# Optimization experiments

Hardware: AMD Instinct MI355X
Metric: run time of the kernel (lower is better)

The kernel has to match this reference:

```python
import jax, jax.numpy as jnp
import numpy as np

COMMITMENT_WEIGHT = 0.25


def setup_inputs() -> dict:
    key = jax.random.key(0)
    k1, k2 = jax.random.split(key)
    embed_dim, codebook_size = 512, 16
    z = jax.random.normal(k1, (8, 8192, embed_dim), dtype=jnp.float32)
    # init matches nn.init.uniform_(-1/K, 1/K) scale; values are arbitrary for correctness testing
    codebook = jax.random.uniform(k2, (codebook_size, embed_dim), dtype=jnp.float32,
                                  minval=-1.0 / codebook_size, maxval=1.0 / codebook_size)
    return {"z": z, "codebook": codebook}


def reference(z, codebook):
    D = z.shape[-1]
    flat_z = z.reshape(-1, D)                                   # [N, D]
    # squared L2 distances via expansion: |z|^2 - 2 z.C^T + |c|^2   -> [N, K]
    distances = (jnp.sum(flat_z * flat_z, axis=1, keepdims=True)
                 - 2.0 * flat_z @ codebook.T
                 + jnp.sum(codebook * codebook, axis=1)[None, :])
    indices = jnp.argmin(distances, axis=1)                      # [N]
    z_q_flat = codebook[indices]                                 # [N, D] gather

    commitment_loss = jnp.mean((flat_z - jax.lax.stop_gradient(z_q_flat)) ** 2)
    codebook_loss = jnp.mean((z_q_flat - jax.lax.stop_gradient(flat_z)) ** 2)
    vq_loss = codebook_loss + COMMITMENT_WEIGHT * commitment_loss

    # straight-through estimator
    z_q_flat = flat_z + jax.lax.stop_gradient(z_q_flat - flat_z)
    z_q = z_q_flat.reshape(z.shape)
    indices = indices.reshape(z.shape[:-1])
    return (z_q, indices, vq_loss)
```

## Files before the change

kernel.cpp:

```cpp
#include <hip/hip_runtime.h>


constexpr int D      = 512;
constexpr int D4     = D / 4;
constexpr int K      = 16;
constexpr int BLOCK  = 256;
constexpr int WAVES  = BLOCK / 64;
constexpr int ROWS_PER_WAVE  = 4;
constexpr int ROWS_PER_BLOCK = WAVES * ROWS_PER_WAVE;
constexpr int GRID   = 2048;

__global__ void __launch_bounds__(BLOCK, 4) vq_kernel(
    const float* __restrict__ z, const float* __restrict__ cb,
    float* __restrict__ zq, float* __restrict__ idx_out,
    float* __restrict__ loss_out, int n_rows, float loss_scale)
{
    __shared__ float cb_lds[K * D];
    __shared__ float cnorm_lds[K];
    __shared__ float wave_loss[WAVES];

    const int tid  = threadIdx.x;
    const int lane = tid & 63;
    const int wave = tid >> 6;
    const int sub  = lane >> 4;
    const int sl   = lane & 15;

    const float4* cb4 = reinterpret_cast<const float4*>(cb);
    float4*       cl4 = reinterpret_cast<float4*>(cb_lds);
    #pragma unroll
    for (int i = 0; i < (K * D4) / BLOCK; ++i)
        cl4[i * BLOCK + tid] = cb4[i * BLOCK + tid];
    __syncthreads();

    {
        const int k = tid >> 4;
        const int s = tid & 15;
        double acc = 0.0;
        #pragma unroll
        for (int i = 0; i < 8; ++i) {
            float4 c = cl4[k * D4 + i * 16 + s];
            acc += (double)c.x * (double)c.x + (double)c.y * (double)c.y
                 + (double)c.z * (double)c.z + (double)c.w * (double)c.w;
        }
        #pragma unroll
        for (int m = 1; m < 16; m <<= 1)
            acc += __shfl_xor(acc, m, 64);
        if (s == 0) cnorm_lds[k] = (float)acc;
    }
    __syncthreads();

    const int base_k = sl & 3;
    float cn[4];
    #pragma unroll
    for (int c = 0; c < 4; ++c) cn[c] = cnorm_lds[4 * c + base_k];

    const float4* z4  = reinterpret_cast<const float4*>(z);
    float4*       zq4 = reinterpret_cast<float4*>(zq);

    float lp = 0.f;

    const int n_tiles = n_rows / ROWS_PER_BLOCK;
    for (int tile = blockIdx.x; tile < n_tiles; tile += GRID) {
        const int row = tile * ROWS_PER_BLOCK + wave * ROWS_PER_WAVE + sub;
        const long long rb = (long long)row * D4;

        float4 zr[8];
        #pragma unroll
        for (int i = 0; i < 8; ++i)
            zr[i] = z4[rb + i * 16 + sl];

        double A = 0.0;
        #pragma unroll
        for (int i = 0; i < 8; ++i) {
            A += (double)zr[i].x * (double)zr[i].x + (double)zr[i].y * (double)zr[i].y
               + (double)zr[i].z * (double)zr[i].z + (double)zr[i].w * (double)zr[i].w;
        }
        #pragma unroll
        for (int m = 1; m < 16; m <<= 1)
            A += __shfl_xor(A, m, 64);
        const float A32 = (float)A;

        float B32[4];
        #pragma unroll
        for (int c = 0; c < 4; ++c) {
            double a0 = 0.0, a1 = 0.0, a2 = 0.0, a3 = 0.0;
            #pragma unroll 1
            for (int i = 0; i < 8; ++i) {
                const int    idx = (4 * c) * D4 + i * 16 + sl;
                const double zx = (double)zr[i].x, zy = (double)zr[i].y;
                const double zz = (double)zr[i].z, zw = (double)zr[i].w;
                float4 c0 = cl4[idx];
                float4 c1 = cl4[idx + D4];
                float4 c2 = cl4[idx + 2 * D4];
                float4 c3 = cl4[idx + 3 * D4];
                a0 = fma((double)c0.x, zx, fma((double)c0.y, zy, fma((double)c0.z, zz, fma((double)c0.w, zw, a0))));
                a1 = fma((double)c1.x, zx, fma((double)c1.y, zy, fma((double)c1.z, zz, fma((double)c1.w, zw, a1))));
                a2 = fma((double)c2.x, zx, fma((double)c2.y, zy, fma((double)c2.z, zz, fma((double)c2.w, zw, a2))));
                a3 = fma((double)c3.x, zx, fma((double)c3.y, zy, fma((double)c3.z, zz, fma((double)c3.w, zw, a3))));
            }
            {
                const int mb0 = lane & 1;
                double s0 = mb0 ? a0 : a1;
                double s1 = mb0 ? a2 : a3;
                double r0 = __shfl_xor(s0, 1, 64);
                double r1 = __shfl_xor(s1, 1, 64);
                double t0 = (mb0 ? a1 : a0) + r0;
                double t1 = (mb0 ? a3 : a2) + r1;
                const int mb1 = (lane >> 1) & 1;
                double s2 = mb1 ? t0 : t1;
                double r2 = __shfl_xor(s2, 2, 64);
                double u  = (mb1 ? t1 : t0) + r2;
                u += __shfl_xor(u, 4, 64);
                u += __shfl_xor(u, 8, 64);
                B32[c] = (float)u;
            }
        }

        float bd = (A32 - 2.0f * B32[0]) + cn[0];
        int   bk = base_k;
        #pragma unroll
        for (int c = 1; c < 4; ++c) {
            float d = (A32 - 2.0f * B32[c]) + cn[c];
            if (d < bd) { bd = d; bk = 4 * c + base_k; }
        }
        #pragma unroll
        for (int b = 0; b < 2; ++b) {
            float od = __shfl_xor(bd, 1 << b, 64);
            int   ok = __shfl_xor(bk, 1 << b, 64);
            if (od < bd || (od == bd && ok < bk)) { bd = od; bk = ok; }
        }
        if (sl == 0) idx_out[row] = (float)bk;

        #pragma unroll
        for (int i = 0; i < 8; ++i) {
            float4 c = cl4[bk * D4 + i * 16 + sl];
            zq4[rb + i * 16 + sl] = c;
            float dx = zr[i].x - c.x, dy = zr[i].y - c.y;
            float dz = zr[i].z - c.z, dw = zr[i].w - c.w;
            lp += dx * dx + dy * dy + dz * dz + dw * dw;
        }
    }

    #pragma unroll
    for (int m = 1; m < 64; m <<= 1)
        lp += __shfl_xor(lp, m, 64);
    if (lane == 0) wave_loss[wave] = lp;
    __syncthreads();
    if (tid == 0) {
        float s = 0.f;
        #pragma unroll
        for (int w = 0; w < WAVES; ++w) s += wave_loss[w];
        atomicAdd(loss_out, s * loss_scale);
    }
}

extern "C" void kernel_launch(void* const* d_in, const int* in_sizes, int n_in,
                              void* d_out, int out_size, void* d_ws, size_t ws_size,
                              hipStream_t stream) {
    const float* z  = (const float*)d_in[0];
    const float* cb = (const float*)d_in[1];

    const int n_elems = in_sizes[0];
    const int n_rows  = n_elems / D;

    float* zq   = (float*)d_out;
    float* idx  = zq + n_elems;
    float* loss = idx + n_rows;

    hipMemsetAsync((void*)loss, 0, sizeof(float), stream);

    const float loss_scale = 1.25f / (float)n_elems;
    vq_kernel<<<GRID, BLOCK, 0, stream>>>(z, cb, zq, idx, loss, n_rows, loss_scale);
}
```

Baseline: 326.9 us.

## Use nontemporal loads/stores, per-wave norms, and drop block-level sync

Switches z loads and zq stores to nontemporal builtins so streaming traffic bypasses cache retention. Each wave now computes codebook norms itself and spreads them with shuffles, removing a shared array and one barrier. The final loss is added with one atomic per wave instead of a block reduction, and the dot-product loop unroll is raised to 2 with launch bounds raised to 5. The costs are four times more loss atomics and redundant norm work in every wave. Higher occupancy may not be reachable given the 32KB LDS per block.

```diff
diff --git a/kernel.cpp b/kernel.cpp
--- a/kernel.cpp
+++ b/kernel.cpp
@@ -1,23 +1,21 @@
 #include <hip/hip_runtime.h>
 
+
+typedef float f32x4 __attribute__((ext_vector_type(4)));
 
 constexpr int D      = 512;
 constexpr int D4     = D / 4;
 constexpr int K      = 16;
 constexpr int BLOCK  = 256;
-constexpr int WAVES  = BLOCK / 64;
-constexpr int ROWS_PER_WAVE  = 4;
-constexpr int ROWS_PER_BLOCK = WAVES * ROWS_PER_WAVE;
+constexpr int ROWS_PER_BLOCK = 16;
 constexpr int GRID   = 2048;
 
-__global__ void __launch_bounds__(BLOCK, 4) vq_kernel(
+__global__ void __launch_bounds__(BLOCK, 5) vq_kernel(
     const float* __restrict__ z, const float* __restrict__ cb,
     float* __restrict__ zq, float* __restrict__ idx_out,
     float* __restrict__ loss_out, int n_rows, float loss_scale)
 {
-    __shared__ float cb_lds[K * D];
-    __shared__ float cnorm_lds[K];
-    __shared__ float wave_loss[WAVES];
+    __shared__ f32x4 cb_lds4[K * D4];
 
     const int tid  = threadIdx.x;
     const int lane = tid & 63;
@@ -25,55 +23,54 @@
     const int sub  = lane >> 4;
     const int sl   = lane & 15;
 
-    const float4* cb4 = reinterpret_cast<const float4*>(cb);
-    float4*       cl4 = reinterpret_cast<float4*>(cb_lds);
+    const f32x4* cb4 = reinterpret_cast<const f32x4*>(cb);
     #pragma unroll
     for (int i = 0; i < (K * D4) / BLOCK; ++i)
-        cl4[i * BLOCK + tid] = cb4[i * BLOCK + tid];
+        cb_lds4[i * BLOCK + tid] = cb4[i * BLOCK + tid];
     __syncthreads();
 
+    float cn[4];
     {
-        const int k = tid >> 4;
-        const int s = tid & 15;
-        double acc = 0.0;
+        const int k_ = lane >> 2;
+        const int s_ = lane & 3;
+        double nacc = 0.0;
+        #pragma unroll 1
+        for (int j = 0; j < 32; ++j) {
+            const int jj = (j + 2 * k_) & 31;
+            f32x4 c = cb_lds4[k_ * D4 + jj * 4 + s_];
+            nacc += (double)c[0] * (double)c[0] + (double)c[1] * (double)c[1]
+                  + (double)c[2] * (double)c[2] + (double)c[3] * (double)c[3];
+        }
+        nacc += __shfl_xor(nacc, 1, 64);
+        nacc += __shfl_xor(nacc, 2, 64);
+        const float normf = (float)nacc;
+        const int base_k = sl & 3;
         #pragma unroll
-        for (int i = 0; i < 8; ++i) {
-            float4 c = cl4[k * D4 + i * 16 + s];
-            acc += (double)c.x * (double)c.x + (double)c.y * (double)c.y
-                 + (double)c.z * (double)c.z + (double)c.w * (double)c.w;
-        }
-        #pragma unroll
-        for (int m = 1; m < 16; m <<= 1)
-            acc += __shfl_xor(acc, m, 64);
-        if (s == 0) cnorm_lds[k] = (float)acc;
+        for (int c = 0; c < 4; ++c)
+            cn[c] = __shfl(normf, (4 * c + base_k) * 4, 64);
     }
-    __syncthreads();
+    const int base_k = sl & 3;
 
-    const int base_k = sl & 3;
-    float cn[4];
-    #pragma unroll
-    for (int c = 0; c < 4; ++c) cn[c] = cnorm_lds[4 * c + base_k];
-
-    const float4* z4  = reinterpret_cast<const float4*>(z);
-    float4*       zq4 = reinterpret_cast<float4*>(zq);
+    const f32x4* z4  = reinterpret_cast<const f32x4*>(z);
+    f32x4*       zq4 = reinterpret_cast<f32x4*>(zq);
 
     float lp = 0.f;
 
     const int n_tiles = n_rows / ROWS_PER_BLOCK;
     for (int tile = blockIdx.x; tile < n_tiles; tile += GRID) {
-        const int row = tile * ROWS_PER_BLOCK + wave * ROWS_PER_WAVE + sub;
+        const int row = tile * ROWS_PER_BLOCK + wave * 4 + sub;
         const long long rb = (long long)row * D4;
 
-        float4 zr[8];
+        f32x4 zr[8];
         #pragma unroll
         for (int i = 0; i < 8; ++i)
-            zr[i] = z4[rb + i * 16 + sl];
+            zr[i] = __builtin_nontemporal_load(&z4[rb + i * 16 + sl]);
 
         double A = 0.0;
         #pragma unroll
         for (int i = 0; i < 8; ++i) {
-            A += (double)zr[i].x * (double)zr[i].x + (double)zr[i].y * (double)zr[i].y
-               + (double)zr[i].z * (double)zr[i].z + (double)zr[i].w * (double)zr[i].w;
+            A += (double)zr[i][0] * (double)zr[i][0] + (double)zr[i][1] * (double)zr[i][1]
+               + (double)zr[i][2] * (double)zr[i][2] + (double)zr[i][3] * (double)zr[i][3];
         }
         #pragma unroll
         for (int m = 1; m < 16; m <<= 1)
@@ -84,19 +81,19 @@
         #pragma unroll
         for (int c = 0; c < 4; ++c) {
             double a0 = 0.0, a1 = 0.0, a2 = 0.0, a3 = 0.0;
-            #pragma unroll 1
+            #pragma unroll 2
             for (int i = 0; i < 8; ++i) {
                 const int    idx = (4 * c) * D4 + i * 16 + sl;
-                const double zx = (double)zr[i].x, zy = (double)zr[i].y;
-                const double zz = (double)zr[i].z, zw = (double)zr[i].w;
-                float4 c0 = cl4[idx];
-                float4 c1 = cl4[idx + D4];
-                float4 c2 = cl4[idx + 2 * D4];
-                float4 c3 = cl4[idx + 3 * D4];
-                a0 = fma((double)c0.x, zx, fma((double)c0.y, zy, fma((double)c0.z, zz, fma((double)c0.w, zw, a0))));
-                a1 = fma((double)c1.x, zx, fma((double)c1.y, zy, fma((double)c1.z, zz, fma((double)c1.w, zw, a1))));
-                a2 = fma((double)c2.x, zx, fma((double)c2.y, zy, fma((double)c2.z, zz, fma((double)c2.w, zw, a2))));
-                a3 = fma((double)c3.x, zx, fma((double)c3.y, zy, fma((double)c3.z, zz, fma((double)c3.w, zw, a3))));
+                const double zx = (double)zr[i][0], zy = (double)zr[i][1];
+                const double zz = (double)zr[i][2], zw = (double)zr[i][3];
+                f32x4 c0 = cb_lds4[idx];
+                f32x4 c1 = cb_lds4[idx + D4];
+                f32x4 c2 = cb_lds4[idx + 2 * D4];
+                f32x4 c3 = cb_lds4[idx + 3 * D4];
+                a0 = fma((double)c0[0], zx, fma((double)c0[1], zy, fma((double)c0[2], zz, fma((double)c0[3], zw, a0))));
+                a1 = fma((double)c1[0], zx, fma((double)c1[1], zy, fma((double)c1[2], zz, fma((double)c1[3], zw, a1))));
+                a2 = fma((double)c2[0], zx, fma((double)c2[1], zy, fma((double)c2[2], zz, fma((double)c2[3], zw, a2))));
+                a3 = fma((double)c3[0], zx, fma((double)c3[1], zy, fma((double)c3[2], zz, fma((double)c3[3], zw, a3))));
             }
             {
                 const int mb0 = lane & 1;
@@ -133,10 +130,10 @@
 
         #pragma unroll
         for (int i = 0; i < 8; ++i) {
-            float4 c = cl4[bk * D4 + i * 16 + sl];
-            zq4[rb + i * 16 + sl] = c;
-            float dx = zr[i].x - c.x, dy = zr[i].y - c.y;
-            float dz = zr[i].z - c.z, dw = zr[i].w - c.w;
+            f32x4 c = cb_lds4[bk * D4 + i * 16 + sl];
+            __builtin_nontemporal_store(c, &zq4[rb + i * 16 + sl]);
+            float dx = zr[i][0] - c[0], dy = zr[i][1] - c[1];
+            float dz = zr[i][2] - c[2], dw = zr[i][3] - c[3];
             lp += dx * dx + dy * dy + dz * dz + dw * dw;
         }
     }
@@ -144,14 +141,8 @@
     #pragma unroll
     for (int m = 1; m < 64; m <<= 1)
         lp += __shfl_xor(lp, m, 64);
-    if (lane == 0) wave_loss[wave] = lp;
-    __syncthreads();
-    if (tid == 0) {
-        float s = 0.f;
-        #pragma unroll
-        for (int w = 0; w < WAVES; ++w) s += wave_loss[w];
-        atomicAdd(loss_out, s * loss_scale);
-    }
+    if (lane == 0)
+        atomicAdd(loss_out, lp * loss_scale);
 }
 
 extern "C" void kernel_launch(void* const* d_in, const int* in_sizes, int n_in,
```

Result: slower. 371.6 us (+13.7%).
